# Kernel tuning notes

Hardware: AMD Instinct MI355X
Metric: run time of the kernel (lower is better)

## Reference

```python
import jax, jax.numpy as jnp
import numpy as np

QMIN, QMAX = -128.0, 127.0


def setup_inputs() -> dict:
    key = jax.random.key(0)
    k1, k2, k3 = jax.random.split(key, 3)
    x = jax.random.normal(k1, (8, 32, 32, 32), jnp.float32)          # NCHW
    weight = jax.random.normal(k2, (32, 32, 3, 3), jnp.float32) * 0.1  # OIHW
    bias = jax.random.normal(k3, (32,), jnp.float32) * 0.01
    # lut[i, j] = (i - 128) * (j - 128), indexed by (q + 128).
    i = jnp.arange(256, dtype=jnp.float32) - 128.0
    lut = i[:, None] * i[None, :]
    return {"x": x, "weight": weight, "bias": bias, "lut": lut}


def reference(x, weight, bias, lut):
    # dynamic per-tensor scales (qmethod = ('dynamic','tensor','tensor'))
    sf = jax.lax.stop_gradient(jnp.max(jnp.abs(x)) / 127.0)
    sw = jax.lax.stop_gradient(jnp.max(jnp.abs(weight)) / 127.0)

    qx = jnp.clip(jnp.round(x / sf), QMIN, QMAX)        # int8 values as float
    qw = jnp.clip(jnp.round(weight / sw), QMIN, QMAX)

    # STE fake-quant tensors (forward = dequant, backward = identity)
    x_fq = x + jax.lax.stop_gradient(qx * sf - x)
    w_fq = weight + jax.lax.stop_gradient(qw * sw - weight)

    pad = ((1, 1), (1, 1))
    conv_fq = jax.lax.conv_general_dilated(
        x_fq, w_fq, window_strides=(1, 1), padding=pad,
        dimension_numbers=('NCHW', 'OIHW', 'NCHW'))

    # ---- LUT-based int8 conv path (forward value) ----
    # im2col on the int8 activation codes; zero padding -> q=0 -> index 128,
    # and lut[128, :] == 0, matching zero-padded conv.
    patches = jax.lax.conv_general_dilated_patches(
        qx, filter_shape=(3, 3), window_strides=(1, 1), padding=pad)
    N, K, Hp, Wp = patches.shape                       # K = Cin*kh*kw
    O = qw.shape[0]
    ix = (patches + 128.0).astype(jnp.int32).reshape(N, K, Hp * Wp)
    ix = jnp.transpose(ix, (0, 2, 1))                  # [N, P, K]
    iw = (qw.reshape(O, K) + 128.0).astype(jnp.int32)  # [O, K]

    # gather approximate products and accumulate over the window
    prods = lut[ix[:, :, None, :], iw[None, None, :, :]]  # [N, P, O, K]
    out_lut = (sf * sw) * jnp.sum(prods, axis=-1)          # [N, P, O]
    out_lut = jnp.transpose(out_lut, (0, 2, 1)).reshape(N, O, Hp, Wp)

    b = bias[None, :, None, None]
    out_fq = conv_fq + b
    out_lut = out_lut + b
    # forward returns the LUT result; gradients flow through the fake-quant conv (STE)
    return out_fq + jax.lax.stop_gradient(out_lut - out_fq)
```

## Files before the change

### kernel.cpp

```cpp
#include <hip/hip_runtime.h>

#define X_N 262144
#define W_N 9216
#define QX_PER_N (34*34*32)
#define QX_BYTES (8*QX_PER_N)
#define QX_INT4 (QX_BYTES/16)

static __device__ __forceinline__ int dot4(int a, int b, int acc) {
#if defined(__has_builtin)
#if __has_builtin(__builtin_amdgcn_sdot4)
  return __builtin_amdgcn_sdot4(a, b, acc, false);
#define DOT4_DONE 1
#endif
#endif
#ifndef DOT4_DONE
  #pragma unroll
  for (int k = 0; k < 4; k++)
    acc += ((a >> (8*k)) << 24 >> 24) * ((b >> (8*k)) << 24 >> 24);
  return acc;
#endif
}

__global__ __launch_bounds__(256) void k_partial_max(
    const float4* __restrict__ x4, const float4* __restrict__ w4,
    float* __restrict__ partials, int4* __restrict__ qx_zero) {
  int b = blockIdx.x, t = threadIdx.x;
  if (b >= 66) {
    for (int i = (b - 66) * 256 + t; i < QX_INT4; i += 8 * 256)
      qx_zero[i] = make_int4(0, 0, 0, 0);
    return;
  }
  __shared__ float red[256];
  float m = 0.f;
  if (b < 64) {
    #pragma unroll
    for (int k = 0; k < 4; k++) {
      float4 v = x4[b * 1024 + k * 256 + t];
      m = fmaxf(m, fmaxf(fmaxf(fabsf(v.x), fabsf(v.y)), fmaxf(fabsf(v.z), fabsf(v.w))));
    }
  } else {
    for (int i = (b - 64) * 256 + t; i < W_N / 4; i += 2 * 256) {
      float4 v = w4[i];
      m = fmaxf(m, fmaxf(fmaxf(fabsf(v.x), fabsf(v.y)), fmaxf(fabsf(v.z), fabsf(v.w))));
    }
  }
  red[t] = m;
  __syncthreads();
  #pragma unroll
  for (int s = 128; s >= 1; s >>= 1) {
    if (t < s) red[t] = fmaxf(red[t], red[t + s]);
    __syncthreads();
  }
  if (t == 0) partials[b] = red[0];
}

__global__ __launch_bounds__(256) void k_finalize_qw(
    const float* __restrict__ w, const float* __restrict__ partials,
    float* __restrict__ sfsw, signed char* __restrict__ qw_r) {
  __shared__ float red[64];
  __shared__ float s_sw;
  int t = threadIdx.x;
  if (t < 64) red[t] = partials[t];
  __syncthreads();
  if (t < 32) red[t] = fmaxf(red[t], red[t + 32]);
  __syncthreads();
  if (t < 16) red[t] = fmaxf(red[t], red[t + 16]);
  __syncthreads();
  if (t < 8) red[t] = fmaxf(red[t], red[t + 8]);
  __syncthreads();
  if (t == 0) {
    float mx = red[0];
    for (int i = 1; i < 8; i++) mx = fmaxf(mx, red[i]);
    float mw = fmaxf(partials[64], partials[65]);
    float sf = mx / 127.f;
    float sw = mw / 127.f;
    sfsw[0] = sf;
    sfsw[1] = sw;
    s_sw = sw;
  }
  __syncthreads();
  float sw = s_sw;
  for (int i = t; i < W_N; i += 256) {
    int o = i / 288, rem = i % 288;
    int c = rem / 9, k9 = rem % 9;
    float r = rintf(w[i] / sw);
    r = fminf(fmaxf(r, -128.f), 127.f);
    qw_r[(o * 9 + k9) * 32 + c] = (signed char)(int)r;
  }
}

__global__ __launch_bounds__(256) void k_quant_x(
    const float* __restrict__ x, const float* __restrict__ sfsw,
    signed char* __restrict__ qx) {
  int p = blockIdx.x * 256 + threadIdx.x;
  int n = p >> 10, hw = p & 1023;
  int h = hw >> 5, w = hw & 31;
  float inv_sf = 1.f / sfsw[0];
  int q[8];
  #pragma unroll
  for (int g = 0; g < 8; g++) {
    int packed = 0;
    #pragma unroll
    for (int j = 0; j < 4; j++) {
      int c = g * 4 + j;
      float v = x[n * 32768 + c * 1024 + hw];
      float r = fminf(fmaxf(rintf(v * inv_sf), -128.f), 127.f);
      packed |= ((int)r & 0xff) << (8 * j);
    }
    q[g] = packed;
  }
  int4* dst = (int4*)(qx + n * QX_PER_N + ((h + 1) * 34 + (w + 1)) * 32);
  dst[0] = make_int4(q[0], q[1], q[2], q[3]);
  dst[1] = make_int4(q[4], q[5], q[6], q[7]);
}

__global__ __launch_bounds__(256) void k_conv(
    const signed char* __restrict__ qx, const signed char* __restrict__ qw_r,
    const float* __restrict__ bias, const float* __restrict__ sfsw,
    float* __restrict__ out) {
  int b = blockIdx.x;
  int strip = b & 3;
  int o = (b >> 2) & 31;
  int n = b >> 7;
  int t = threadIdx.x;
  int h = strip * 8 + (t >> 5);
  int w = t & 31;

  const signed char* qxn = qx + n * QX_PER_N;
  const int* wq = (const int*)qw_r + o * 72;

  int acc = 0;
  #pragma unroll
  for (int ky = 0; ky < 3; ky++) {
    const int4* row = (const int4*)(qxn + ((h + ky) * 34 + w) * 32);
    int4 p0 = row[0], p1 = row[1], p2 = row[2], p3 = row[3], p4 = row[4], p5 = row[5];
    const int* wr = wq + ky * 24;
    acc = dot4(p0.x, wr[0],  acc); acc = dot4(p0.y, wr[1],  acc);
    acc = dot4(p0.z, wr[2],  acc); acc = dot4(p0.w, wr[3],  acc);
    acc = dot4(p1.x, wr[4],  acc); acc = dot4(p1.y, wr[5],  acc);
    acc = dot4(p1.z, wr[6],  acc); acc = dot4(p1.w, wr[7],  acc);
    acc = dot4(p2.x, wr[8],  acc); acc = dot4(p2.y, wr[9],  acc);
    acc = dot4(p2.z, wr[10], acc); acc = dot4(p2.w, wr[11], acc);
    acc = dot4(p3.x, wr[12], acc); acc = dot4(p3.y, wr[13], acc);
    acc = dot4(p3.z, wr[14], acc); acc = dot4(p3.w, wr[15], acc);
    acc = dot4(p4.x, wr[16], acc); acc = dot4(p4.y, wr[17], acc);
    acc = dot4(p4.z, wr[18], acc); acc = dot4(p4.w, wr[19], acc);
    acc = dot4(p5.x, wr[20], acc); acc = dot4(p5.y, wr[21], acc);
    acc = dot4(p5.z, wr[22], acc); acc = dot4(p5.w, wr[23], acc);
  }

  float scale = sfsw[0] * sfsw[1];
  out[(n * 32 + o) * 1024 + h * 32 + w] = scale * (float)acc + bias[o];
}

extern "C" void kernel_launch(void* const* d_in, const int* in_sizes, int n_in,
                              void* d_out, int out_size, void* d_ws, size_t ws_size,
                              hipStream_t stream) {
  const float* x    = (const float*)d_in[0];
  const float* w    = (const float*)d_in[1];
  const float* bias = (const float*)d_in[2];
  float* out = (float*)d_out;

  char* ws = (char*)d_ws;
  float*       partials = (float*)(ws + 0);
  float*       sfsw     = (float*)(ws + 1024);
  signed char* qw_r     = (signed char*)(ws + 2048);
  signed char* qx       = (signed char*)(ws + 16384);

  k_partial_max<<<74, 256, 0, stream>>>((const float4*)x, (const float4*)w,
                                        partials, (int4*)qx);
  k_finalize_qw<<<1, 256, 0, stream>>>(w, partials, sfsw, qw_r);
  k_quant_x<<<32, 256, 0, stream>>>(x, sfsw, qx);
  k_conv<<<1024, 256, 0, stream>>>(qx, qw_r, bias, sfsw, out);
}
```

Baseline: 75.01 us.

## Fuse activation quantization into conv via shared-memory tiles and atomic max scale

Cuts the pipeline from four kernels to two. The x max-abs reduction now ends in a global atomicMax on float bits, which removes the separate finalize kernel; the weight block quantizes and reorders the weights itself. Each conv block quantizes its own padded 10x34 activation tile into shared memory, which removes the padded qx buffer, its zero-fill and the quant kernel. The costs are redundant quantization of the same tile by every output-channel block and an atomic max slot that is never reset in the code, so it relies on the workspace starting at zero.

```diff
diff --git a/kernel.cpp b/kernel.cpp
--- a/kernel.cpp
+++ b/kernel.cpp
@@ -1,10 +1,6 @@
 #include <hip/hip_runtime.h>
 
-#define X_N 262144
 #define W_N 9216
-#define QX_PER_N (34*34*32)
-#define QX_BYTES (8*QX_PER_N)
-#define QX_INT4 (QX_BYTES/16)
 
 static __device__ __forceinline__ int dot4(int a, int b, int acc) {
 #if defined(__has_builtin)
@@ -21,16 +17,13 @@
 #endif
 }
 
-__global__ __launch_bounds__(256) void k_partial_max(
+__global__ __launch_bounds__(256) void k_scales(
     const float4* __restrict__ x4, const float4* __restrict__ w4,
-    float* __restrict__ partials, int4* __restrict__ qx_zero) {
+    int* __restrict__ xmax_bits, float* __restrict__ sw_out,
+    signed char* __restrict__ qw_r) {
+  __shared__ float red[256];
+  __shared__ float s_sw;
   int b = blockIdx.x, t = threadIdx.x;
-  if (b >= 66) {
-    for (int i = (b - 66) * 256 + t; i < QX_INT4; i += 8 * 256)
-      qx_zero[i] = make_int4(0, 0, 0, 0);
-    return;
-  }
-  __shared__ float red[256];
   float m = 0.f;
   if (b < 64) {
     #pragma unroll
@@ -39,7 +32,7 @@
       m = fmaxf(m, fmaxf(fmaxf(fabsf(v.x), fabsf(v.y)), fmaxf(fabsf(v.z), fabsf(v.w))));
     }
   } else {
-    for (int i = (b - 64) * 256 + t; i < W_N / 4; i += 2 * 256) {
+    for (int i = t; i < W_N / 4; i += 256) {
       float4 v = w4[i];
       m = fmaxf(m, fmaxf(fmaxf(fabsf(v.x), fabsf(v.y)), fmaxf(fabsf(v.z), fabsf(v.w))));
     }
@@ -51,35 +44,18 @@
     if (t < s) red[t] = fmaxf(red[t], red[t + s]);
     __syncthreads();
   }
-  if (t == 0) partials[b] = red[0];
-}
-
-__global__ __launch_bounds__(256) void k_finalize_qw(
-    const float* __restrict__ w, const float* __restrict__ partials,
-    float* __restrict__ sfsw, signed char* __restrict__ qw_r) {
-  __shared__ float red[64];
-  __shared__ float s_sw;
-  int t = threadIdx.x;
-  if (t < 64) red[t] = partials[t];
-  __syncthreads();
-  if (t < 32) red[t] = fmaxf(red[t], red[t + 32]);
-  __syncthreads();
-  if (t < 16) red[t] = fmaxf(red[t], red[t + 16]);
-  __syncthreads();
-  if (t < 8) red[t] = fmaxf(red[t], red[t + 8]);
-  __syncthreads();
+  if (b < 64) {
+    if (t == 0) atomicMax(xmax_bits, __float_as_int(red[0]));
+    return;
+  }
   if (t == 0) {
-    float mx = red[0];
-    for (int i = 1; i < 8; i++) mx = fmaxf(mx, red[i]);
-    float mw = fmaxf(partials[64], partials[65]);
-    float sf = mx / 127.f;
-    float sw = mw / 127.f;
-    sfsw[0] = sf;
-    sfsw[1] = sw;
+    float sw = red[0] / 127.f;
+    sw_out[0] = sw;
     s_sw = sw;
   }
   __syncthreads();
   float sw = s_sw;
+  const float* w = (const float*)w4;
   for (int i = t; i < W_N; i += 256) {
     int o = i / 288, rem = i % 288;
     int c = rem / 9, k9 = rem % 9;
@@ -89,68 +65,59 @@
   }
 }
 
-__global__ __launch_bounds__(256) void k_quant_x(
-    const float* __restrict__ x, const float* __restrict__ sfsw,
-    signed char* __restrict__ qx) {
-  int p = blockIdx.x * 256 + threadIdx.x;
-  int n = p >> 10, hw = p & 1023;
-  int h = hw >> 5, w = hw & 31;
-  float inv_sf = 1.f / sfsw[0];
-  int q[8];
-  #pragma unroll
-  for (int g = 0; g < 8; g++) {
-    int packed = 0;
-    #pragma unroll
-    for (int j = 0; j < 4; j++) {
-      int c = g * 4 + j;
-      float v = x[n * 32768 + c * 1024 + hw];
-      float r = fminf(fmaxf(rintf(v * inv_sf), -128.f), 127.f);
-      packed |= ((int)r & 0xff) << (8 * j);
-    }
-    q[g] = packed;
-  }
-  int4* dst = (int4*)(qx + n * QX_PER_N + ((h + 1) * 34 + (w + 1)) * 32);
-  dst[0] = make_int4(q[0], q[1], q[2], q[3]);
-  dst[1] = make_int4(q[4], q[5], q[6], q[7]);
-}
-
-__global__ __launch_bounds__(256) void k_conv(
-    const signed char* __restrict__ qx, const signed char* __restrict__ qw_r,
-    const float* __restrict__ bias, const float* __restrict__ sfsw,
-    float* __restrict__ out) {
+__global__ __launch_bounds__(256, 4) void k_conv(
+    const float* __restrict__ x, const signed char* __restrict__ qw_r,
+    const float* __restrict__ bias, const int* __restrict__ xmax_bits,
+    const float* __restrict__ sw_in, float* __restrict__ out) {
   int b = blockIdx.x;
   int strip = b & 3;
   int o = (b >> 2) & 31;
   int n = b >> 7;
   int t = threadIdx.x;
-  int h = strip * 8 + (t >> 5);
-  int w = t & 31;
 
-  const signed char* qxn = qx + n * QX_PER_N;
+  __shared__ int ts[8 * 10 * 34];
+
+  float sf = __int_as_float(xmax_bits[0]) / 127.f;
+  float inv_sf = 1.f / sf;
+  const float* xn = x + n * 32768;
+
+  for (int idx = t; idx < 2720; idx += 256) {
+    int g = idx / 340, s = idx % 340;
+    int r = s / 34, cc = s % 34;
+    int gh = strip * 8 - 1 + r;
+    int gw = cc - 1;
+    int packed = 0;
+    if ((unsigned)gh < 32u && (unsigned)gw < 32u) {
+      const float* p = xn + g * 4096 + gh * 32 + gw;
+      #pragma unroll
+      for (int j = 0; j < 4; j++) {
+        float r1 = fminf(fmaxf(rintf(p[j * 1024] * inv_sf), -128.f), 127.f);
+        packed |= ((int)r1 & 0xff) << (8 * j);
+      }
+    }
+    ts[idx] = packed;
+  }
+  __syncthreads();
+
+  int row = t >> 5, col = t & 31;
   const int* wq = (const int*)qw_r + o * 72;
 
   int acc = 0;
   #pragma unroll
-  for (int ky = 0; ky < 3; ky++) {
-    const int4* row = (const int4*)(qxn + ((h + ky) * 34 + w) * 32);
-    int4 p0 = row[0], p1 = row[1], p2 = row[2], p3 = row[3], p4 = row[4], p5 = row[5];
-    const int* wr = wq + ky * 24;
-    acc = dot4(p0.x, wr[0],  acc); acc = dot4(p0.y, wr[1],  acc);
-    acc = dot4(p0.z, wr[2],  acc); acc = dot4(p0.w, wr[3],  acc);
-    acc = dot4(p1.x, wr[4],  acc); acc = dot4(p1.y, wr[5],  acc);
-    acc = dot4(p1.z, wr[6],  acc); acc = dot4(p1.w, wr[7],  acc);
-    acc = dot4(p2.x, wr[8],  acc); acc = dot4(p2.y, wr[9],  acc);
-    acc = dot4(p2.z, wr[10], acc); acc = dot4(p2.w, wr[11], acc);
-    acc = dot4(p3.x, wr[12], acc); acc = dot4(p3.y, wr[13], acc);
-    acc = dot4(p3.z, wr[14], acc); acc = dot4(p3.w, wr[15], acc);
-    acc = dot4(p4.x, wr[16], acc); acc = dot4(p4.y, wr[17], acc);
-    acc = dot4(p4.z, wr[18], acc); acc = dot4(p4.w, wr[19], acc);
-    acc = dot4(p5.x, wr[20], acc); acc = dot4(p5.y, wr[21], acc);
-    acc = dot4(p5.z, wr[22], acc); acc = dot4(p5.w, wr[23], acc);
+  for (int g = 0; g < 8; g++) {
+    const int* tg = ts + g * 340;
+    #pragma unroll
+    for (int ky = 0; ky < 3; ky++) {
+      const int* tr = tg + (row + ky) * 34 + col;
+      acc = dot4(tr[0], wq[(ky * 3 + 0) * 8 + g], acc);
+      acc = dot4(tr[1], wq[(ky * 3 + 1) * 8 + g], acc);
+      acc = dot4(tr[2], wq[(ky * 3 + 2) * 8 + g], acc);
+    }
   }
 
-  float scale = sfsw[0] * sfsw[1];
-  out[(n * 32 + o) * 1024 + h * 32 + w] = scale * (float)acc + bias[o];
+  float scale = sf * sw_in[0];
+  int h = strip * 8 + row;
+  out[(n * 32 + o) * 1024 + h * 32 + col] = scale * (float)acc + bias[o];
 }
 
 extern "C" void kernel_launch(void* const* d_in, const int* in_sizes, int n_in,
@@ -161,15 +128,12 @@
   const float* bias = (const float*)d_in[2];
   float* out = (float*)d_out;
 
-  char* ws = (char*)d_ws;
-  float*       partials = (float*)(ws + 0);
-  float*       sfsw     = (float*)(ws + 1024);
-  signed char* qw_r     = (signed char*)(ws + 2048);
-  signed char* qx       = (signed char*)(ws + 16384);
+  char* wsb = (char*)d_ws;
+  int*         xmax_bits = (int*)(wsb + 0);
+  float*       sw_out    = (float*)(wsb + 64);
+  signed char* qw_r      = (signed char*)(wsb + 2048);
 
-  k_partial_max<<<74, 256, 0, stream>>>((const float4*)x, (const float4*)w,
-                                        partials, (int4*)qx);
-  k_finalize_qw<<<1, 256, 0, stream>>>(w, partials, sfsw, qw_r);
-  k_quant_x<<<32, 256, 0, stream>>>(x, sfsw, qx);
-  k_conv<<<1024, 256, 0, stream>>>(qx, qw_r, bias, sfsw, out);
+  k_scales<<<65, 256, 0, stream>>>((const float4*)x, (const float4*)w,
+                                   xmax_bits, sw_out, qw_r);
+  k_conv<<<1024, 256, 0, stream>>>(x, qw_r, bias, xmax_bits, sw_out, out);
 }
```

Result: slower. 78.71 us (+4.9%).
